# Kernel optimization log

Measured on AMD Instinct MI355X. Metric: run time of the kernel, lower is better.

## Reference

```python
import jax, jax.numpy as jnp
import numpy as np

# einspline cubic B-spline basis matrix (4x4)
BASIS = jnp.array([[-1.0, 3.0, -3.0, 1.0],
                   [ 3.0, -6.0, 0.0, 4.0],
                   [-3.0, 3.0, 3.0, 1.0],
                   [ 1.0, 0.0, 0.0, 0.0]], dtype=jnp.float32) / 6.0


def _build_1d_system_matrix(M: int) -> jnp.ndarray:
    """(M+2, M+2) natural-boundary interpolating B-spline system matrix."""
    delta = 1.0 / (M - 1)
    dinv2 = (1.0 / delta) ** 2
    A = np.zeros((M + 2, M + 2), dtype=np.float32)
    A[0, 0] = dinv2; A[0, 1] = -2.0 * dinv2; A[0, 2] = dinv2
    i = np.arange(1, M + 1)
    A[i, i - 1] = 1.0 / 6.0
    A[i, i] = 2.0 / 3.0
    A[i, i + 1] = 1.0 / 6.0
    A[M + 1, M - 1] = dinv2; A[M + 1, M] = -2.0 * dinv2; A[M + 1, M + 1] = dinv2
    return jnp.asarray(A)


def find_coefs_2d(data: jnp.ndarray) -> jnp.ndarray:
    """data: (C, Mx, My) -> coefs: (C, Mx+2, My+2) via separable solves."""
    C, Mx, My = data.shape
    Ax = _build_1d_system_matrix(Mx)
    Ay = _build_1d_system_matrix(My)
    # solve along x for every (c, y)
    d = jnp.transpose(data, (0, 2, 1)).reshape(-1, Mx)          # (C*My, Mx)
    Bx = jnp.zeros((d.shape[0], Mx + 2), dtype=data.dtype).at[:, 1:Mx + 1].set(d)
    cx = jnp.linalg.solve(Ax, Bx.T).T                           # (C*My, Mx+2)
    cx = jnp.transpose(cx.reshape(C, My, Mx + 2), (0, 2, 1))    # (C, Mx+2, My)
    # solve along y for every (c, x)
    d2 = cx.reshape(-1, My)                                      # (C*(Mx+2), My)
    By = jnp.zeros((d2.shape[0], My + 2), dtype=data.dtype).at[:, 1:My + 1].set(d2)
    coefs = jnp.linalg.solve(Ay, By.T).T.reshape(C, Mx + 2, My + 2)
    return coefs


def _axis_index(un: jnp.ndarray, M: int):
    """Cell index + local fraction with out-of-range extrapolation handling."""
    i = jnp.floor(un).astype(jnp.int32)
    t = un - i.astype(un.dtype)
    low = un < 0
    i = jnp.where(low, 0, i)
    t = jnp.where(low, un, t)
    high = un >= M - 2
    i = jnp.where(high, M - 2, i)
    t = jnp.where(high, un - (M - 2), t)
    return i, t


def interpolate_grid_2d(coefs: jnp.ndarray, u: jnp.ndarray) -> jnp.ndarray:
    """coefs: (C, Mx+2, My+2); u: (B, 2) in [0,1]^2 -> (B, C)."""
    C, Mxp2, Myp2 = coefs.shape
    Mx, My = Mxp2 - 2, Myp2 - 2
    ux_norm = u[:, 0] * (Mx - 1)
    uy_norm = u[:, 1] * (My - 1)
    ix, tx = _axis_index(ux_norm, Mx)
    iy, ty = _axis_index(uy_norm, My)
    ones = jnp.ones_like(tx)
    tx_powers = jnp.stack([tx ** 3, tx ** 2, tx, ones], axis=0)  # (4, B)
    ty_powers = jnp.stack([ty ** 3, ty ** 2, ty, ones], axis=0)  # (4, B)
    basis_x = BASIS @ tx_powers                                   # (4, B)
    basis_y = BASIS @ ty_powers                                   # (4, B)
    offsets = jnp.arange(4, dtype=jnp.int32)
    ix_exp = ix[None, :] + offsets[:, None]                       # (4, B)
    iy_exp = iy[None, :] + offsets[:, None]                       # (4, B)
    # 4x4 neighborhood gather: (C, 4, 4, B)
    control_grid = coefs[:, ix_exp[:, None, :], iy_exp[None, :, :]]
    intermediate = jnp.einsum('cijb,ib->cjb', control_grid, basis_x)
    values = jnp.einsum('cjb,jb->cb', intermediate, basis_y)
    return values.T                                               # (B, C)


def setup_inputs() -> dict:
    key = jax.random.key(0)
    k_u, k_d = jax.random.split(key)
    u = jax.random.uniform(k_u, (2000000, 2), dtype=jnp.float32)
    data = jax.random.normal(k_d, (4, 64, 64), dtype=jnp.float32)
    return {"u": u, "data": data}


def reference(u, data):
    coefs = find_coefs_2d(data)
    return interpolate_grid_2d(coefs, u)
```

## Files before the change

### kernel.cpp

```cpp
#include <hip/hip_runtime.h>
#include <math.h>

#define MX 64
#define NC 4
#define NI 66
#define NINT 62

typedef _Float16 half4  __attribute__((ext_vector_type(4)));
typedef _Float16 half2v __attribute__((ext_vector_type(2)));

struct TC { float m[NINT]; float inv[NINT]; };
constexpr TC make_tc() {
    TC tc{};
    double dp = 2.0/3.0;
    tc.m[0] = 0.0f;
    tc.inv[0] = (float)(1.0/dp);
    for (int j = 1; j < NINT; ++j) {
        double m = (1.0/6.0) / dp;
        tc.m[j] = (float)m;
        dp = 2.0/3.0 - m*(1.0/6.0);
        tc.inv[j] = (float)(1.0/dp);
    }
    return tc;
}
__constant__ constexpr TC g_tc = make_tc();

__global__ __launch_bounds__(256) void solve_fused(const float* __restrict__ data,
                                                   float4* __restrict__ coefsOut)
{
    __shared__ float cxS[NC][NI][65];
    __shared__ half4 chS[NI*NI];
    const int t = threadIdx.x;
    const float a = 1.0f/6.0f;

    {
        const int c = t >> 6, y = t & 63;
        const float* g = data + c*(MX*MX) + y;
        float w[NINT];
        const float d0 = g[0];
        const float dM = g[63*MX];
        w[0] = g[1*MX] - a*d0;
        #pragma unroll
        for (int j = 1; j < NINT; ++j) {
            float r = g[(j+1)*MX];
            if (j == NINT-1) r -= a*dM;
            w[j] = r - g_tc.m[j]*w[j-1];
        }
        float x = w[NINT-1] * g_tc.inv[NINT-1];
        const float c63 = x;
        cxS[c][63][y] = x;
        #pragma unroll
        for (int j = NINT-2; j >= 0; --j) {
            x = (w[j] - a*x) * g_tc.inv[j];
            cxS[c][j+2][y] = x;
        }
        cxS[c][0][y]  = 2.0f*d0 - x;
        cxS[c][1][y]  = d0;
        cxS[c][64][y] = dM;
        cxS[c][65][y] = 2.0f*dM - c63;
    }
    __syncthreads();

    for (int line = t; line < NC*NI; line += 256) {
        const int c = line / NI;
        const int i = line - c*NI;
        const float* g = &cxS[c][i][0];
        _Float16* o = ((_Float16*)&chS[i*NI]) + c;

        float w[NINT];
        const float d0 = g[0];
        const float dM = g[63];
        w[0] = g[1] - a*d0;
        #pragma unroll
        for (int j = 1; j < NINT; ++j) {
            float r = g[j+1];
            if (j == NINT-1) r -= a*dM;
            w[j] = r - g_tc.m[j]*w[j-1];
        }
        float x = w[NINT-1] * g_tc.inv[NINT-1];
        const float c63 = x;
        o[63*NC] = (_Float16)x;
        #pragma unroll
        for (int j = NINT-2; j >= 0; --j) {
            x = (w[j] - a*x) * g_tc.inv[j];
            o[(j+2)*NC] = (_Float16)x;
        }
        o[0*NC]  = (_Float16)(2.0f*d0 - x);
        o[1*NC]  = (_Float16)d0;
        o[64*NC] = (_Float16)dM;
        o[65*NC] = (_Float16)(2.0f*dM - c63);
    }
    __syncthreads();

    const float4* src = (const float4*)chS;
    for (int s = t; s < (NI*NI)/2; s += 256) coefsOut[s] = src[s];
}

__device__ __forceinline__ float4 eval_pt(const half4* __restrict__ lds,
                                          float ux, float uy)
{
    const float unx = ux * 63.0f;
    const float uny = uy * 63.0f;

    int ix = (int)unx; ix = ix > 62 ? 62 : ix; ix = ix < 0 ? 0 : ix;
    int iy = (int)uny; iy = iy > 62 ? 62 : iy; iy = iy < 0 ? 0 : iy;
    const float tx = unx - (float)ix;
    const float ty = uny - (float)iy;

    const half2v t = __builtin_bit_cast(half2v, __builtin_amdgcn_cvt_pkrtz(tx, ty));
    const half2v c16  = half2v{(_Float16)(1.0f/6.0f), (_Float16)(1.0f/6.0f)};
    const half2v ch   = half2v{(_Float16)0.5f,  (_Float16)0.5f};
    const half2v cnh  = half2v{(_Float16)-0.5f, (_Float16)-0.5f};
    const half2v cn16 = half2v{(_Float16)(-1.0f/6.0f), (_Float16)(-1.0f/6.0f)};
    const half2v cn1  = half2v{(_Float16)-1.0f, (_Float16)-1.0f};
    const half2v c23  = half2v{(_Float16)(2.0f/3.0f), (_Float16)(2.0f/3.0f)};

    const half2v t2 = t*t;
    half2v b0 = (cn16*t + ch)*t;  b0 = (b0 + cnh)*t + c16;
    half2v b1 = (ch*t + cn1)*t2 + c23;
    half2v b2 = (cnh*t + ch)*t;   b2 = (b2 + ch)*t + c16;
    half2v b3 = c16*(t*t2);

    const half2v by0 = __builtin_shufflevector(b0, b0, 1, 1);
    const half2v by1 = __builtin_shufflevector(b1, b1, 1, 1);
    const half2v by2 = __builtin_shufflevector(b2, b2, 1, 1);
    const half2v by3 = __builtin_shufflevector(b3, b3, 1, 1);
    const half2v bx[4] = {
        __builtin_shufflevector(b0, b0, 0, 0),
        __builtin_shufflevector(b1, b1, 0, 0),
        __builtin_shufflevector(b2, b2, 0, 0),
        __builtin_shufflevector(b3, b3, 0, 0),
    };

    const half4* r = lds + (ix*NI + iy);
    half2v t01, t23;
    #pragma unroll
    for (int ar = 0; ar < 4; ++ar) {
        const half4 c0 = r[ar*NI + 0];
        const half4 c1 = r[ar*NI + 1];
        const half4 c2 = r[ar*NI + 2];
        const half4 c3 = r[ar*NI + 3];
        half2v a01 = c0.lo*by0 + c1.lo*by1 + c2.lo*by2 + c3.lo*by3;
        half2v a23 = c0.hi*by0 + c1.hi*by1 + c2.hi*by2 + c3.hi*by3;
        if (ar == 0) { t01 = a01*bx[0];        t23 = a23*bx[0]; }
        else         { t01 = a01*bx[ar] + t01; t23 = a23*bx[ar] + t23; }
    }
    return make_float4((float)t01.x, (float)t01.y, (float)t23.x, (float)t23.y);
}

__global__ __launch_bounds__(512, 8) void interp(const float2* __restrict__ u,
                                                 const half4* __restrict__ coefsH,
                                                 float4* __restrict__ out, int B)
{
    __shared__ half4 lds[NI*NI];
    for (int s = threadIdx.x; s < NI*NI; s += 512) lds[s] = coefsH[s];
    __syncthreads();

    const int stride = gridDim.x * 512;
    for (int p = blockIdx.x*512 + threadIdx.x; p < B; p += stride) {
        const float2 uv = u[p];
        out[p] = eval_pt(lds, uv.x, uv.y);
    }
}

extern "C" void kernel_launch(void* const* d_in, const int* in_sizes, int n_in,
                              void* d_out, int out_size, void* d_ws, size_t ws_size,
                              hipStream_t stream)
{
    const float* u    = (const float*)d_in[0];
    const float* data = (const float*)d_in[1];
    const int B = in_sizes[0] / 2;

    float4* coefsQ = (float4*)d_ws;

    solve_fused<<<1, 256, 0, stream>>>(data, coefsQ);
    interp<<<1024, 512, 0, stream>>>((const float2*)u, (const half4*)coefsQ,
                                     (float4*)d_out, B);
}
```

Baseline: 88.66 us.

## Fuse spline coefficient solve into interpolation kernel, recomputing per block

Removes the separate single-block solve kernel and the workspace round trip. Every interpolation block now recomputes the 2D coefficient table into shared memory itself, two channels at a time, before evaluating its points. This trades a kernel launch and a serial dependency for redundant per-block solve work, which lengthens each block's prologue, and the launch bound changes from 8 to 4 blocks.

```diff
diff --git a/kernel.cpp b/kernel.cpp
--- a/kernel.cpp
+++ b/kernel.cpp
@@ -24,77 +24,6 @@
     return tc;
 }
 __constant__ constexpr TC g_tc = make_tc();
-
-__global__ __launch_bounds__(256) void solve_fused(const float* __restrict__ data,
-                                                   float4* __restrict__ coefsOut)
-{
-    __shared__ float cxS[NC][NI][65];
-    __shared__ half4 chS[NI*NI];
-    const int t = threadIdx.x;
-    const float a = 1.0f/6.0f;
-
-    {
-        const int c = t >> 6, y = t & 63;
-        const float* g = data + c*(MX*MX) + y;
-        float w[NINT];
-        const float d0 = g[0];
-        const float dM = g[63*MX];
-        w[0] = g[1*MX] - a*d0;
-        #pragma unroll
-        for (int j = 1; j < NINT; ++j) {
-            float r = g[(j+1)*MX];
-            if (j == NINT-1) r -= a*dM;
-            w[j] = r - g_tc.m[j]*w[j-1];
-        }
-        float x = w[NINT-1] * g_tc.inv[NINT-1];
-        const float c63 = x;
-        cxS[c][63][y] = x;
-        #pragma unroll
-        for (int j = NINT-2; j >= 0; --j) {
-            x = (w[j] - a*x) * g_tc.inv[j];
-            cxS[c][j+2][y] = x;
-        }
-        cxS[c][0][y]  = 2.0f*d0 - x;
-        cxS[c][1][y]  = d0;
-        cxS[c][64][y] = dM;
-        cxS[c][65][y] = 2.0f*dM - c63;
-    }
-    __syncthreads();
-
-    for (int line = t; line < NC*NI; line += 256) {
-        const int c = line / NI;
-        const int i = line - c*NI;
-        const float* g = &cxS[c][i][0];
-        _Float16* o = ((_Float16*)&chS[i*NI]) + c;
-
-        float w[NINT];
-        const float d0 = g[0];
-        const float dM = g[63];
-        w[0] = g[1] - a*d0;
-        #pragma unroll
-        for (int j = 1; j < NINT; ++j) {
-            float r = g[j+1];
-            if (j == NINT-1) r -= a*dM;
-            w[j] = r - g_tc.m[j]*w[j-1];
-        }
-        float x = w[NINT-1] * g_tc.inv[NINT-1];
-        const float c63 = x;
-        o[63*NC] = (_Float16)x;
-        #pragma unroll
-        for (int j = NINT-2; j >= 0; --j) {
-            x = (w[j] - a*x) * g_tc.inv[j];
-            o[(j+2)*NC] = (_Float16)x;
-        }
-        o[0*NC]  = (_Float16)(2.0f*d0 - x);
-        o[1*NC]  = (_Float16)d0;
-        o[64*NC] = (_Float16)dM;
-        o[65*NC] = (_Float16)(2.0f*dM - c63);
-    }
-    __syncthreads();
-
-    const float4* src = (const float4*)chS;
-    for (int s = t; s < (NI*NI)/2; s += 256) coefsOut[s] = src[s];
-}
 
 __device__ __forceinline__ float4 eval_pt(const half4* __restrict__ lds,
                                           float ux, float uy)
@@ -148,18 +77,81 @@
     return make_float4((float)t01.x, (float)t01.y, (float)t23.x, (float)t23.y);
 }
 
-__global__ __launch_bounds__(512, 8) void interp(const float2* __restrict__ u,
-                                                 const half4* __restrict__ coefsH,
-                                                 float4* __restrict__ out, int B)
+__global__ __launch_bounds__(512, 4) void fused(const float* __restrict__ data,
+                                                const float2* __restrict__ u,
+                                                float4* __restrict__ out, int B)
 {
-    __shared__ half4 lds[NI*NI];
-    for (int s = threadIdx.x; s < NI*NI; s += 512) lds[s] = coefsH[s];
-    __syncthreads();
+    __shared__ float cxS[2][NI][65];
+    __shared__ half4 tab[NI*NI];
+    const int t = threadIdx.x;
+    const float a = 1.0f/6.0f;
+
+    #pragma unroll
+    for (int cc = 0; cc < 2; ++cc) {
+        if (t < 128) {
+            const int c2 = t >> 6, y = t & 63;
+            const float* g = data + (cc*2 + c2)*(MX*MX) + y;
+            float w[NINT];
+            const float d0 = g[0];
+            const float dM = g[63*MX];
+            w[0] = g[1*MX] - a*d0;
+            #pragma unroll
+            for (int j = 1; j < NINT; ++j) {
+                float r = g[(j+1)*MX];
+                if (j == NINT-1) r -= a*dM;
+                w[j] = r - g_tc.m[j]*w[j-1];
+            }
+            float x = w[NINT-1] * g_tc.inv[NINT-1];
+            const float c63 = x;
+            cxS[c2][63][y] = x;
+            #pragma unroll
+            for (int j = NINT-2; j >= 0; --j) {
+                x = (w[j] - a*x) * g_tc.inv[j];
+                cxS[c2][j+2][y] = x;
+            }
+            cxS[c2][0][y]  = 2.0f*d0 - x;
+            cxS[c2][1][y]  = d0;
+            cxS[c2][64][y] = dM;
+            cxS[c2][65][y] = 2.0f*dM - c63;
+        }
+        __syncthreads();
+
+        if (t < 2*NI) {
+            const int c2 = t < NI ? 0 : 1;
+            const int i  = t - c2*NI;
+            const float* g = &cxS[c2][i][0];
+            _Float16* o = ((_Float16*)&tab[i*NI]) + (cc*2 + c2);
+
+            float w[NINT];
+            const float d0 = g[0];
+            const float dM = g[63];
+            w[0] = g[1] - a*d0;
+            #pragma unroll
+            for (int j = 1; j < NINT; ++j) {
+                float r = g[j+1];
+                if (j == NINT-1) r -= a*dM;
+                w[j] = r - g_tc.m[j]*w[j-1];
+            }
+            float x = w[NINT-1] * g_tc.inv[NINT-1];
+            const float c63 = x;
+            o[63*NC] = (_Float16)x;
+            #pragma unroll
+            for (int j = NINT-2; j >= 0; --j) {
+                x = (w[j] - a*x) * g_tc.inv[j];
+                o[(j+2)*NC] = (_Float16)x;
+            }
+            o[0*NC]  = (_Float16)(2.0f*d0 - x);
+            o[1*NC]  = (_Float16)d0;
+            o[64*NC] = (_Float16)dM;
+            o[65*NC] = (_Float16)(2.0f*dM - c63);
+        }
+        __syncthreads();
+    }
 
     const int stride = gridDim.x * 512;
-    for (int p = blockIdx.x*512 + threadIdx.x; p < B; p += stride) {
+    for (int p = blockIdx.x*512 + t; p < B; p += stride) {
         const float2 uv = u[p];
-        out[p] = eval_pt(lds, uv.x, uv.y);
+        out[p] = eval_pt(tab, uv.x, uv.y);
     }
 }
 
@@ -171,9 +163,5 @@
     const float* data = (const float*)d_in[1];
     const int B = in_sizes[0] / 2;
 
-    float4* coefsQ = (float4*)d_ws;
-
-    solve_fused<<<1, 256, 0, stream>>>(data, coefsQ);
-    interp<<<1024, 512, 0, stream>>>((const float2*)u, (const half4*)coefsQ,
-                                     (float4*)d_out, B);
+    fused<<<1024, 512, 0, stream>>>(data, (const float2*)u, (float4*)d_out, B);
 }
```

Measured after the change: 91.76 us. 3.5% more time.
